# Kernel optimization log

Hardware: AMD Instinct MI355X
Metric: run time of the kernel (lower is better)

## Reference

```python
import jax, jax.numpy as jnp
import numpy as np

N_NODES = 100_000
N_EDGES = 1_600_000
D_IN = 128
D_HID = 128
LN_EPS = 1e-5


def setup_inputs() -> dict:
    key = jax.random.key(0)
    k1, k2, k3 = jax.random.split(key, 3)
    x = jax.random.normal(k1, (N_NODES, D_IN), dtype=jnp.float32)
    edge_index = jax.random.randint(k2, (2, N_EDGES), 0, N_NODES, dtype=jnp.int32)
    # GCNConv linear weight (glorot-ish) and bias
    W = jax.random.normal(k3, (D_IN, D_HID), dtype=jnp.float32) * (1.0 / np.sqrt(D_IN))
    b = jnp.zeros((D_HID,), dtype=jnp.float32)
    # LayerNorm params
    gamma = jnp.ones((D_HID,), dtype=jnp.float32)
    beta = jnp.zeros((D_HID,), dtype=jnp.float32)
    return {"x": x, "edge_index": edge_index, "W": W, "b": b, "gamma": gamma, "beta": beta}


def reference(x, edge_index, W, b, gamma, beta):
    n = x.shape[0]
    # --- GCNConv: add self-loops, symmetric normalization ---
    loop = jnp.arange(n, dtype=edge_index.dtype)
    row = jnp.concatenate([edge_index[0], loop])  # source j
    col = jnp.concatenate([edge_index[1], loop])  # target i
    deg = jax.ops.segment_sum(jnp.ones(row.shape, x.dtype), col, num_segments=n)
    dinv = jnp.where(deg > 0, jax.lax.rsqrt(deg), jnp.zeros_like(deg))
    norm = dinv[row] * dinv[col]  # [E+N]
    # transform first (input->hidden), then gather-scale-scatter
    h = x @ W  # [N, D_HID]
    msg = h[row] * norm[:, None]  # gather + per-edge scale
    out = jax.ops.segment_sum(msg, col, num_segments=n) + b  # scatter-add
    # --- LayerNorm ---
    mu = jnp.mean(out, axis=-1, keepdims=True)
    var = jnp.mean(jnp.square(out - mu), axis=-1, keepdims=True)
    ln = (out - mu) * jax.lax.rsqrt(var + LN_EPS) * gamma + beta
    # Dropout is identity at inference; ReLU
    return jax.nn.relu(ln)
```

## Files before the change

kernel.cpp:

```cpp
#include <hip/hip_runtime.h>
#include <hip/hip_bf16.h>
#include <math.h>

#define LN_EPS 1e-5f
#define CAP 8192
#define CAPSH 13

typedef __attribute__((ext_vector_type(8))) short short8;
typedef __attribute__((ext_vector_type(4))) float floatx4;

__global__ __launch_bounds__(256) void k_partition(const int* __restrict__ ei, int* __restrict__ bucketCnt,
                                                   unsigned* __restrict__ pk, int E, int chunk) {
    __shared__ int ecol[3328];
    __shared__ int esrc[3328];
    __shared__ int h[512];
    __shared__ int base[512];
    int t = threadIdx.x;
    for (int i = t; i < 512; i += 256) h[i] = 0;
    int e0 = blockIdx.x * chunk;
    int e1 = min(e0 + chunk, E);
    int n = e1 - e0;
    __syncthreads();
    for (int i = t; i < n; i += 256) {
        int col = ei[E + e0 + i];
        ecol[i] = col;
        esrc[i] = ei[e0 + i];
        atomicAdd(&h[col >> 8], 1);
    }
    __syncthreads();
    for (int i = t; i < 512; i += 256) {
        if (h[i] > 0) {
            base[i] = atomicAdd(&bucketCnt[i], h[i]);
            h[i] = 0;
        }
    }
    __syncthreads();
    for (int i = t; i < n; i += 256) {
        int col = ecol[i];
        int b = col >> 8;
        int r = base[b] + atomicAdd(&h[b], 1);
        if (r < CAP)
            pk[((unsigned)b << CAPSH) + r] = ((unsigned)(col & 255) << 20) | (unsigned)esrc[i];
    }
}

__global__ __launch_bounds__(256) void k_csr(const unsigned* __restrict__ pk, const int* __restrict__ bucketCnt,
                                             int* __restrict__ cnt, int* __restrict__ rowptr,
                                             float* __restrict__ dinv, int* __restrict__ srcidx, int N) {
    __shared__ int lcnt[256];
    __shared__ int lofs[256];
    __shared__ int s[256];
    int b = blockIdx.x;
    int t = threadIdx.x;
    int ofs = b << CAPSH;
    int cntb = min(bucketCnt[b], CAP);
    lcnt[t] = 0;
    __syncthreads();
    for (int e = t; e < cntb; e += 256)
        atomicAdd(&lcnt[pk[ofs + e] >> 20], 1);
    __syncthreads();
    int v = lcnt[t];
    s[t] = v;
    __syncthreads();
    int val = v;
    for (int off = 1; off < 256; off <<= 1) {
        int add = (t >= off) ? s[t - off] : 0;
        __syncthreads();
        val += add;
        s[t] = val;
        __syncthreads();
    }
    lofs[t] = val - v;
    int node = (b << 8) + t;
    if (node < N) {
        cnt[node] = v;
        rowptr[node] = ofs + lofs[t];
        dinv[node] = rsqrtf((float)(v + 1));
    }
    lcnt[t] = 0;
    __syncthreads();
    for (int e = t; e < cntb; e += 256) {
        unsigned pv = pk[ofs + e];
        int d = pv >> 20;
        int r = atomicAdd(&lcnt[d], 1);
        srcidx[ofs + lofs[d] + r] = (int)(pv & 0xFFFFFu);
    }
}

__global__ __launch_bounds__(256) void k_cvtW(const float* __restrict__ W, __hip_bfloat16* __restrict__ Wt) {
    int i = blockIdx.x * 256 + threadIdx.x;
    int n = i >> 7, k = i & 127;
    Wt[i] = __float2bfloat16(W[k * 128 + n]);
}

__global__ __launch_bounds__(256) void k_gemm(const float* __restrict__ x, const __hip_bfloat16* __restrict__ Wt,
                                              const float* __restrict__ dinv, __hip_bfloat16* __restrict__ g, int N) {
    __shared__ unsigned short sA[128 * 128];
    __shared__ unsigned short sB[128 * 128];
    int tid = threadIdx.x;
    int row0 = blockIdx.x * 128;
#pragma unroll
    for (int i = 0; i < 8; ++i) {
        int idx = tid + i * 256;
        int row = idx >> 4;
        int gr = idx & 15;
        int arow = min(row0 + row, N - 1);
        float4 xa = *(const float4*)(x + (size_t)arow * 128 + gr * 8);
        float4 xb = *(const float4*)(x + (size_t)arow * 128 + gr * 8 + 4);
        union { short8 s; __hip_bfloat16 h[8]; } a;
        a.h[0] = __float2bfloat16(xa.x); a.h[1] = __float2bfloat16(xa.y);
        a.h[2] = __float2bfloat16(xa.z); a.h[3] = __float2bfloat16(xa.w);
        a.h[4] = __float2bfloat16(xb.x); a.h[5] = __float2bfloat16(xb.y);
        a.h[6] = __float2bfloat16(xb.z); a.h[7] = __float2bfloat16(xb.w);
        int grs = gr ^ (row & 15);
        *(short8*)(&sA[row * 128 + grs * 8]) = a.s;
        *(short8*)(&sB[row * 128 + grs * 8]) = *(const short8*)(Wt + (size_t)row * 128 + gr * 8);
    }
    __syncthreads();
    int lane = tid & 63;
    int wv = tid >> 6;
    int m = lane & 15;
    int q = lane >> 4;
    floatx4 acc[2][8];
#pragma unroll
    for (int mt = 0; mt < 2; ++mt)
#pragma unroll
        for (int nt = 0; nt < 8; ++nt) acc[mt][nt] = (floatx4){0.f, 0.f, 0.f, 0.f};
#pragma unroll
    for (int kc = 0; kc < 4; ++kc) {
        int gg = kc * 4 + q;
        short8 afrag[2], bfrag[8];
#pragma unroll
        for (int mt = 0; mt < 2; ++mt) {
            int row = wv * 32 + mt * 16 + m;
            afrag[mt] = *(const short8*)(&sA[row * 128 + (gg ^ (row & 15)) * 8]);
        }
#pragma unroll
        for (int nt = 0; nt < 8; ++nt) {
            int n = nt * 16 + m;
            bfrag[nt] = *(const short8*)(&sB[n * 128 + (gg ^ (n & 15)) * 8]);
        }
#pragma unroll
        for (int mt = 0; mt < 2; ++mt)
#pragma unroll
            for (int nt = 0; nt < 8; ++nt)
                acc[mt][nt] = __builtin_amdgcn_mfma_f32_16x16x32_bf16(afrag[mt], bfrag[nt], acc[mt][nt], 0, 0, 0);
    }
#pragma unroll
    for (int mt = 0; mt < 2; ++mt) {
#pragma unroll
        for (int i = 0; i < 4; ++i) {
            int row = row0 + wv * 32 + mt * 16 + q * 4 + i;
            if (row < N) {
                float dv = dinv[row];
                __hip_bfloat16* gp = g + (size_t)row * 128;
#pragma unroll
                for (int nt = 0; nt < 8; ++nt)
                    gp[nt * 16 + m] = __float2bfloat16(acc[mt][nt][i] * dv);
            }
        }
    }
}

__global__ __launch_bounds__(256) void k_agg_ln(const __hip_bfloat16* __restrict__ g, const int* __restrict__ srcidx,
                                                const int* __restrict__ rowptr, const int* __restrict__ cnt,
                                                const float* __restrict__ dinv, const float* __restrict__ bias,
                                                const float* __restrict__ gamma, const float* __restrict__ beta,
                                                float* __restrict__ out, int N) {
    int wid = (int)((blockIdx.x * 256u + threadIdx.x) >> 6);
    int lane = threadIdx.x & 63;
    if (wid >= N) return;
    const unsigned* g1 = (const unsigned*)g;
    unsigned sv = g1[(size_t)wid * 64 + lane];
    float ax = __uint_as_float(sv << 16);
    float ay = __uint_as_float(sv & 0xFFFF0000u);
    int start = rowptr[wid];
    int end = start + cnt[wid];
    int e = start;
    for (; e + 8 <= end; e += 8) {
        int j0 = srcidx[e],     j1 = srcidx[e + 1], j2 = srcidx[e + 2], j3 = srcidx[e + 3];
        int j4 = srcidx[e + 4], j5 = srcidx[e + 5], j6 = srcidx[e + 6], j7 = srcidx[e + 7];
        unsigned v0 = g1[(size_t)j0 * 64 + lane];
        unsigned v1 = g1[(size_t)j1 * 64 + lane];
        unsigned v2 = g1[(size_t)j2 * 64 + lane];
        unsigned v3 = g1[(size_t)j3 * 64 + lane];
        unsigned v4 = g1[(size_t)j4 * 64 + lane];
        unsigned v5 = g1[(size_t)j5 * 64 + lane];
        unsigned v6 = g1[(size_t)j6 * 64 + lane];
        unsigned v7 = g1[(size_t)j7 * 64 + lane];
        ax += ((__uint_as_float(v0 << 16) + __uint_as_float(v1 << 16)) +
               (__uint_as_float(v2 << 16) + __uint_as_float(v3 << 16))) +
              ((__uint_as_float(v4 << 16) + __uint_as_float(v5 << 16)) +
               (__uint_as_float(v6 << 16) + __uint_as_float(v7 << 16)));
        ay += ((__uint_as_float(v0 & 0xFFFF0000u) + __uint_as_float(v1 & 0xFFFF0000u)) +
               (__uint_as_float(v2 & 0xFFFF0000u) + __uint_as_float(v3 & 0xFFFF0000u))) +
              ((__uint_as_float(v4 & 0xFFFF0000u) + __uint_as_float(v5 & 0xFFFF0000u)) +
               (__uint_as_float(v6 & 0xFFFF0000u) + __uint_as_float(v7 & 0xFFFF0000u)));
    }
    for (; e < end; ++e) {
        unsigned v = g1[(size_t)srcidx[e] * 64 + lane];
        ax += __uint_as_float(v << 16);
        ay += __uint_as_float(v & 0xFFFF0000u);
    }
    float di = dinv[wid];
    int c0 = lane * 2;
    float vx = ax * di + bias[c0];
    float vy = ay * di + bias[c0 + 1];
    float sum = vx + vy, sq = vx * vx + vy * vy;
#pragma unroll
    for (int off = 32; off > 0; off >>= 1) {
        sum += __shfl_xor(sum, off, 64);
        sq += __shfl_xor(sq, off, 64);
    }
    float mu = sum * (1.0f / 128.0f);
    float var = sq * (1.0f / 128.0f) - mu * mu;
    float rstd = rsqrtf(var + LN_EPS);
    float o0 = fmaxf((vx - mu) * rstd * gamma[c0] + beta[c0], 0.f);
    float o1 = fmaxf((vy - mu) * rstd * gamma[c0 + 1] + beta[c0 + 1], 0.f);
    ((float2*)out)[(size_t)wid * 64 + lane] = make_float2(o0, o1);
}

extern "C" void kernel_launch(void* const* d_in, const int* in_sizes, int n_in,
                              void* d_out, int out_size, void* d_ws, size_t ws_size,
                              hipStream_t stream) {
    const float* x = (const float*)d_in[0];
    const int* ei = (const int*)d_in[1];
    const float* W = (const float*)d_in[2];
    const float* bias = (const float*)d_in[3];
    const float* gamma = (const float*)d_in[4];
    const float* beta = (const float*)d_in[5];
    float* out = (float*)d_out;

    int N = in_sizes[0] / 128;
    int E = in_sizes[1] / 2;
    int NBUCK = (N + 255) / 256;

    char* p = (char*)d_ws;
    auto alloc = [&](size_t bytes) {
        char* r = p;
        p += (bytes + 255) & ~(size_t)255;
        return r;
    };
    int* cnt = (int*)alloc((size_t)N * 4);
    int* rowptr = (int*)alloc((size_t)N * 4);
    float* dinv = (float*)alloc((size_t)N * 4);
    int* bucketCnt = (int*)alloc(512 * 4);
    __hip_bfloat16* Wt = (__hip_bfloat16*)alloc(128 * 128 * 2);
    int* srcidx = (int*)alloc((size_t)NBUCK * CAP * 4);
    __hip_bfloat16* gbuf = (__hip_bfloat16*)alloc((size_t)N * 128 * 2);
    unsigned* pk = (unsigned*)gbuf;

    const int NBLK = 512;
    int chunk = (E + NBLK - 1) / NBLK;

    hipMemsetAsync(bucketCnt, 0, 512 * 4, stream);
    k_partition<<<NBLK, 256, 0, stream>>>(ei, bucketCnt, pk, E, chunk);
    k_csr<<<NBUCK, 256, 0, stream>>>(pk, bucketCnt, cnt, rowptr, dinv, srcidx, N);
    k_cvtW<<<64, 256, 0, stream>>>(W, Wt);
    k_gemm<<<(N + 127) / 128, 256, 0, stream>>>(x, Wt, dinv, gbuf, N);
    k_agg_ln<<<(N + 3) / 4, 256, 0, stream>>>(gbuf, srcidx, rowptr, cnt, dinv, bias, gamma, beta, out, N);
}
```

Before: 234.8 us.

## Pad CSR rows to multiples of eight, load indices per wave, fold W conversion

```diff
diff --git a/kernel.cpp b/kernel.cpp
--- a/kernel.cpp
+++ b/kernel.cpp
@@ -10,7 +10,15 @@
 typedef __attribute__((ext_vector_type(4))) float floatx4;
 
 __global__ __launch_bounds__(256) void k_partition(const int* __restrict__ ei, int* __restrict__ bucketCnt,
-                                                   unsigned* __restrict__ pk, int E, int chunk) {
+                                                   unsigned* __restrict__ pk, int E, int chunk,
+                                                   const float* __restrict__ W, __hip_bfloat16* __restrict__ Wt) {
+    if (blockIdx.x == gridDim.x - 1) {
+        for (int i = threadIdx.x; i < 16384; i += 256) {
+            int n = i >> 7, k = i & 127;
+            Wt[i] = __float2bfloat16(W[k * 128 + n]);
+        }
+        return;
+    }
     __shared__ int ecol[3328];
     __shared__ int esrc[3328];
     __shared__ int h[512];
@@ -60,9 +68,10 @@
         atomicAdd(&lcnt[pk[ofs + e] >> 20], 1);
     __syncthreads();
     int v = lcnt[t];
-    s[t] = v;
-    __syncthreads();
-    int val = v;
+    int pv = (v + 7) & ~7;
+    s[t] = pv;
+    __syncthreads();
+    int val = pv;
     for (int off = 1; off < 256; off <<= 1) {
         int add = (t >= off) ? s[t - off] : 0;
         __syncthreads();
@@ -70,27 +79,26 @@
         s[t] = val;
         __syncthreads();
     }
-    lofs[t] = val - v;
+    lofs[t] = val - pv;
     int node = (b << 8) + t;
     if (node < N) {
-        cnt[node] = v;
+        cnt[node] = pv;
         rowptr[node] = ofs + lofs[t];
         dinv[node] = rsqrtf((float)(v + 1));
+        for (int i = v; i < pv; ++i) {
+            int slot = lofs[t] + i;
+            if (slot < CAP) srcidx[ofs + slot] = N;
+        }
     }
     lcnt[t] = 0;
     __syncthreads();
     for (int e = t; e < cntb; e += 256) {
-        unsigned pv = pk[ofs + e];
-        int d = pv >> 20;
+        unsigned pvv = pk[ofs + e];
+        int d = pvv >> 20;
         int r = atomicAdd(&lcnt[d], 1);
-        srcidx[ofs + lofs[d] + r] = (int)(pv & 0xFFFFFu);
-    }
-}
-
-__global__ __launch_bounds__(256) void k_cvtW(const float* __restrict__ W, __hip_bfloat16* __restrict__ Wt) {
-    int i = blockIdx.x * 256 + threadIdx.x;
-    int n = i >> 7, k = i & 127;
-    Wt[i] = __float2bfloat16(W[k * 128 + n]);
+        int slot = lofs[d] + r;
+        if (slot < CAP) srcidx[ofs + slot] = (int)(pvv & 0xFFFFFu);
+    }
 }
 
 __global__ __launch_bounds__(256) void k_gemm(const float* __restrict__ x, const __hip_bfloat16* __restrict__ Wt,
@@ -162,6 +170,26 @@
     }
 }
 
+#define LOAD8(P, OFF) \
+    unsigned P##0 = g1[((size_t)(unsigned)__builtin_amdgcn_readlane(myidx, j + OFF + 0)) * 64u + lane]; \
+    unsigned P##1 = g1[((size_t)(unsigned)__builtin_amdgcn_readlane(myidx, j + OFF + 1)) * 64u + lane]; \
+    unsigned P##2 = g1[((size_t)(unsigned)__builtin_amdgcn_readlane(myidx, j + OFF + 2)) * 64u + lane]; \
+    unsigned P##3 = g1[((size_t)(unsigned)__builtin_amdgcn_readlane(myidx, j + OFF + 3)) * 64u + lane]; \
+    unsigned P##4 = g1[((size_t)(unsigned)__builtin_amdgcn_readlane(myidx, j + OFF + 4)) * 64u + lane]; \
+    unsigned P##5 = g1[((size_t)(unsigned)__builtin_amdgcn_readlane(myidx, j + OFF + 5)) * 64u + lane]; \
+    unsigned P##6 = g1[((size_t)(unsigned)__builtin_amdgcn_readlane(myidx, j + OFF + 6)) * 64u + lane]; \
+    unsigned P##7 = g1[((size_t)(unsigned)__builtin_amdgcn_readlane(myidx, j + OFF + 7)) * 64u + lane];
+
+#define ACC8(P) \
+    ax += ((__uint_as_float(P##0 << 16) + __uint_as_float(P##1 << 16)) + \
+           (__uint_as_float(P##2 << 16) + __uint_as_float(P##3 << 16))) + \
+          ((__uint_as_float(P##4 << 16) + __uint_as_float(P##5 << 16)) + \
+           (__uint_as_float(P##6 << 16) + __uint_as_float(P##7 << 16))); \
+    ay += ((__uint_as_float(P##0 & 0xFFFF0000u) + __uint_as_float(P##1 & 0xFFFF0000u)) + \
+           (__uint_as_float(P##2 & 0xFFFF0000u) + __uint_as_float(P##3 & 0xFFFF0000u))) + \
+          ((__uint_as_float(P##4 & 0xFFFF0000u) + __uint_as_float(P##5 & 0xFFFF0000u)) + \
+           (__uint_as_float(P##6 & 0xFFFF0000u) + __uint_as_float(P##7 & 0xFFFF0000u)));
+
 __global__ __launch_bounds__(256) void k_agg_ln(const __hip_bfloat16* __restrict__ g, const int* __restrict__ srcidx,
                                                 const int* __restrict__ rowptr, const int* __restrict__ cnt,
                                                 const float* __restrict__ dinv, const float* __restrict__ bias,
@@ -174,33 +202,23 @@
     unsigned sv = g1[(size_t)wid * 64 + lane];
     float ax = __uint_as_float(sv << 16);
     float ay = __uint_as_float(sv & 0xFFFF0000u);
-    int start = rowptr[wid];
-    int end = start + cnt[wid];
-    int e = start;
-    for (; e + 8 <= end; e += 8) {
-        int j0 = srcidx[e],     j1 = srcidx[e + 1], j2 = srcidx[e + 2], j3 = srcidx[e + 3];
-        int j4 = srcidx[e + 4], j5 = srcidx[e + 5], j6 = srcidx[e + 6], j7 = srcidx[e + 7];
-        unsigned v0 = g1[(size_t)j0 * 64 + lane];
-        unsigned v1 = g1[(size_t)j1 * 64 + lane];
-        unsigned v2 = g1[(size_t)j2 * 64 + lane];
-        unsigned v3 = g1[(size_t)j3 * 64 + lane];
-        unsigned v4 = g1[(size_t)j4 * 64 + lane];
-        unsigned v5 = g1[(size_t)j5 * 64 + lane];
-        unsigned v6 = g1[(size_t)j6 * 64 + lane];
-        unsigned v7 = g1[(size_t)j7 * 64 + lane];
-        ax += ((__uint_as_float(v0 << 16) + __uint_as_float(v1 << 16)) +
-               (__uint_as_float(v2 << 16) + __uint_as_float(v3 << 16))) +
-              ((__uint_as_float(v4 << 16) + __uint_as_float(v5 << 16)) +
-               (__uint_as_float(v6 << 16) + __uint_as_float(v7 << 16)));
-        ay += ((__uint_as_float(v0 & 0xFFFF0000u) + __uint_as_float(v1 & 0xFFFF0000u)) +
-               (__uint_as_float(v2 & 0xFFFF0000u) + __uint_as_float(v3 & 0xFFFF0000u))) +
-              ((__uint_as_float(v4 & 0xFFFF0000u) + __uint_as_float(v5 & 0xFFFF0000u)) +
-               (__uint_as_float(v6 & 0xFFFF0000u) + __uint_as_float(v7 & 0xFFFF0000u)));
-    }
-    for (; e < end; ++e) {
-        unsigned v = g1[(size_t)srcidx[e] * 64 + lane];
-        ax += __uint_as_float(v << 16);
-        ay += __uint_as_float(v & 0xFFFF0000u);
+    int start = __builtin_amdgcn_readfirstlane(rowptr[wid]);
+    int pcnt = __builtin_amdgcn_readfirstlane(cnt[wid]);
+    int end = start + pcnt;
+    for (int eb = start; eb < end; eb += 64) {
+        int myidx = srcidx[eb + lane];
+        int nb = min(64, end - eb);
+        int j = 0;
+        for (; j + 16 <= nb; j += 16) {
+            LOAD8(pa, 0)
+            LOAD8(pb, 8)
+            ACC8(pa)
+            ACC8(pb)
+        }
+        for (; j < nb; j += 8) {
+            LOAD8(pc, 0)
+            ACC8(pc)
+        }
     }
     float di = dinv[wid];
     int c0 = lane * 2;
@@ -246,17 +264,17 @@
     float* dinv = (float*)alloc((size_t)N * 4);
     int* bucketCnt = (int*)alloc(512 * 4);
     __hip_bfloat16* Wt = (__hip_bfloat16*)alloc(128 * 128 * 2);
-    int* srcidx = (int*)alloc((size_t)NBUCK * CAP * 4);
-    __hip_bfloat16* gbuf = (__hip_bfloat16*)alloc((size_t)N * 128 * 2);
+    int* srcidx = (int*)alloc(((size_t)NBUCK * CAP + 64) * 4);
+    __hip_bfloat16* gbuf = (__hip_bfloat16*)alloc((size_t)(N + 1) * 128 * 2);
     unsigned* pk = (unsigned*)gbuf;
 
     const int NBLK = 512;
     int chunk = (E + NBLK - 1) / NBLK;
 
     hipMemsetAsync(bucketCnt, 0, 512 * 4, stream);
-    k_partition<<<NBLK, 256, 0, stream>>>(ei, bucketCnt, pk, E, chunk);
+    hipMemsetAsync(gbuf + (size_t)N * 128, 0, 256, stream);
+    k_partition<<<NBLK + 1, 256, 0, stream>>>(ei, bucketCnt, pk, E, chunk, W, Wt);
     k_csr<<<NBUCK, 256, 0, stream>>>(pk, bucketCnt, cnt, rowptr, dinv, srcidx, N);
-    k_cvtW<<<64, 256, 0, stream>>>(W, Wt);
     k_gemm<<<(N + 127) / 128, 256, 0, stream>>>(x, Wt, dinv, gbuf, N);
     k_agg_ln<<<(N + 3) / 4, 256, 0, stream>>>(gbuf, srcidx, rowptr, cnt, dinv, bias, gamma, beta, out, N);
 }
```

Result: faster. 220.2 us (-6.2%).
